# Kernel tuning notes

Hardware: AMD Instinct MI355X
Metric: run time of the kernel (lower is better)

## Reference

```python
import jax, jax.numpy as jnp
import numpy as np

K = 20  # neighbors
DIM = 1024  # args.dim
NCLS = 13  # args.n_classes


def _knn_idx(xt, k):
    # xt: (B,N,C). Torch computes topk of negative squared distances (self included).
    xx = jnp.sum(xt * xt, axis=-1)                       # (B,N)
    inner = jnp.einsum('bnc,bmc->bnm', xt, xt)           # (B,N,N)
    pd = 2.0 * inner - xx[:, :, None] - xx[:, None, :]   # -||xi-xj||^2
    return jax.lax.top_k(pd, k)[1]                       # (B,N,k) int32


def _graph_feature(xt, k):
    # xt: (B,N,C) -> (B,N,k,2C) = concat(neighbor - center, center)
    idx = _knn_idx(xt, k)
    nbr = jax.vmap(lambda a, i: a[i])(xt, idx)           # (B,N,k,C)
    ctr = jnp.broadcast_to(xt[:, :, None, :], nbr.shape)
    return jnp.concatenate([nbr - ctr, ctr], axis=-1)


def _cbl(x, w, s, b):
    # 1x1 conv (no bias) + folded eval-mode BatchNorm (scale s, bias b) + LeakyReLU(0.2)
    y = jnp.einsum('...c,oc->...o', x, w) * s + b
    return jnp.where(y > 0, y, 0.2 * y)


def setup_inputs() -> dict:
    key = jax.random.key(0)
    ks = iter(jax.random.split(key, 64))
    d = {'x': jax.random.normal(next(ks), (8, 3, 4096), jnp.float32)}
    layers = [('1', 64, 6), ('2', 64, 64), ('3', 64, 128), ('4', 64, 64),
              ('5', 64, 128), ('6', DIM, 192), ('8', 256, DIM + 192),
              ('9', 256, 256), ('10', 128, 256)]
    for name, o, i in layers:
        d['w' + name] = jax.random.normal(next(ks), (o, i), jnp.float32) * (1.0 / np.sqrt(i))
        d['s' + name] = jax.random.uniform(next(ks), (o,), jnp.float32, 0.5, 1.5)
        d['b' + name] = jax.random.normal(next(ks), (o,), jnp.float32) * 0.1
    d['w11'] = jax.random.normal(next(ks), (NCLS, 128), jnp.float32) * (1.0 / np.sqrt(128))
    return d


def reference(x, w1, s1, b1, w2, s2, b2, w3, s3, b3, w4, s4, b4,
              w5, s5, b5, w6, s6, b6, w8, s8, b8, w9, s9, b9,
              w10, s10, b10, w11):
    B, _, N = x.shape
    xt = jnp.transpose(x, (0, 2, 1))                      # (B,N,3)

    f = _graph_feature(xt, K)                             # (B,N,k,6)
    f = _cbl(_cbl(f, w1, s1, b1), w2, s2, b2)
    x1 = jnp.max(f, axis=2)                               # (B,N,64)

    f = _graph_feature(x1, K)                             # (B,N,k,128)
    f = _cbl(_cbl(f, w3, s3, b3), w4, s4, b4)
    x2 = jnp.max(f, axis=2)                               # (B,N,64)

    f = _graph_feature(x2, K)
    f = _cbl(f, w5, s5, b5)
    x3 = jnp.max(f, axis=2)                               # (B,N,64)

    cat = jnp.concatenate([x1, x2, x3], axis=-1)          # (B,N,192)
    g = _cbl(cat, w6, s6, b6)                             # (B,N,DIM)
    g = jnp.broadcast_to(jnp.max(g, axis=1, keepdims=True), (B, N, DIM))

    h = jnp.concatenate([g, x1, x2, x3], axis=-1)         # (B,N,DIM+192)
    h = _cbl(h, w8, s8, b8)                               # dropout is eval-mode identity
    h = _cbl(h, w9, s9, b9)
    h = _cbl(h, w10, s10, b10)
    out = jnp.einsum('bnc,oc->bno', h, w11)               # (B,N,NCLS)
    return jnp.transpose(out, (0, 2, 1))                  # (B,NCLS,N)
```

## Files before the change

### kernel.cpp

```cpp
#include <hip/hip_runtime.h>
#include <cstdint>
#include <cstddef>

#define NPTS 4096
#define BATCH 8
#define KNB 20
#define SLOTS 18
#define FLUSH_THR 3

__device__ __forceinline__ float leaky(float v) { return v > 0.f ? v : 0.2f * v; }

__device__ __forceinline__ unsigned encf(float f) {
  unsigned u = __float_as_uint(f);
  return (u & 0x80000000u) ? ~u : (u | 0x80000000u);
}
__device__ __forceinline__ float decf(unsigned e) {
  unsigned u = (e & 0x80000000u) ? (e & 0x7FFFFFFFu) : ~e;
  return __uint_as_float(u);
}

__device__ __forceinline__ unsigned long long mkkey(float pd, int j) {
  unsigned s = encf(pd);
  return (((unsigned long long)(~s)) << 32) | (unsigned)j;
}

__device__ __forceinline__ void tk_insert(float (&hf)[KNB], int (&hj)[KNB], float pd, int j) {
  if (pd > hf[KNB - 1]) {
    float cf = pd;
    int cj = j;
#pragma unroll
    for (int t = 0; t < KNB; ++t) {
      bool gt = cf > hf[t];
      float nf = gt ? cf : hf[t];
      int nj = gt ? cj : hj[t];
      cf = gt ? hf[t] : cf;
      cj = gt ? hj[t] : cj;
      hf[t] = nf;
      hj[t] = nj;
    }
  }
}

#define NEGINF (__int_as_float(0xff800000))

__device__ __forceinline__ void flushbuf(const float* bpd, const unsigned short* bidx, int t, int& cnt, float& thr,
                                         float (&hf)[KNB], int (&hj)[KNB]) {
  for (int s = 0; s < SLOTS; ++s) {
    if (!__any(s < cnt)) break;
    if (s < cnt) {
      float pd = bpd[s * 256 + t];
      int j = bidx[s * 256 + t];
      tk_insert(hf, hj, pd, j);
    }
  }
  cnt = 0;
  thr = hf[KNB - 1];
}

#define APPEND(PD, J)                        \
  do {                                       \
    float _p = (PD);                         \
    if (_p > thr) {                          \
      bpd[cnt * 256 + t] = _p;               \
      bidx[cnt * 256 + t] = (unsigned short)(J); \
      ++cnt;                                 \
    }                                        \
  } while (0)

__device__ __forceinline__ void merge4_out(unsigned long long* mb, int t, const float (&hf)[KNB], const int (&hj)[KNB],
                                           int* __restrict__ op_base) {
#pragma unroll
  for (int s = 0; s < KNB; ++s) mb[(size_t)t * KNB + s] = mkkey(hf[s], hj[s]);
  __syncthreads();
  if ((t & 3) == 0) {
    int p0 = 0, p1 = 0, p2 = 0, p3 = 0;
    const unsigned long long* l0 = mb + (size_t)(t + 0) * KNB;
    const unsigned long long* l1 = mb + (size_t)(t + 1) * KNB;
    const unsigned long long* l2 = mb + (size_t)(t + 2) * KNB;
    const unsigned long long* l3 = mb + (size_t)(t + 3) * KNB;
    for (int s = 0; s < KNB; ++s) {
      unsigned long long u0 = (p0 < KNB) ? l0[p0] : ~0ULL;
      unsigned long long u1 = (p1 < KNB) ? l1[p1] : ~0ULL;
      unsigned long long u2 = (p2 < KNB) ? l2[p2] : ~0ULL;
      unsigned long long u3 = (p3 < KNB) ? l3[p3] : ~0ULL;
      unsigned long long m01 = u0 < u1 ? u0 : u1;
      int s01 = u0 < u1 ? 0 : 1;
      unsigned long long m23 = u2 < u3 ? u2 : u3;
      int s23 = u2 < u3 ? 2 : 3;
      unsigned long long mm = m01 < m23 ? m01 : m23;
      int sm = m01 < m23 ? s01 : s23;
      p0 += (sm == 0);
      p1 += (sm == 1);
      p2 += (sm == 2);
      p3 += (sm == 3);
      op_base[s] = (int)(mm & 0xFFFFFFFFu);
    }
  }
}

__global__ __launch_bounds__(256) void knn_c3(const float* __restrict__ x, int* __restrict__ idxo) {
  __shared__ float smem[11008];
  float4* f4t = (float4*)smem;
  float* bpd = smem + 4096;
  unsigned short* bidx = (unsigned short*)(smem + 8704);
  int b = blockIdx.y, t = threadIdx.x;
  int q = t >> 2, sub = t & 3;
  int i = blockIdx.x * 64 + q;
  const float* xb = x + (size_t)b * 3 * NPTS;
  float qx = xb[i], qy = xb[NPTS + i], qz = xb[2 * NPTS + i];
  float qn = fmaf(qz, qz, fmaf(qy, qy, qx * qx));
  float hf[KNB];
  int hj[KNB];
#pragma unroll
  for (int s = 0; s < KNB; ++s) {
    hf[s] = NEGINF;
    hj[s] = 0x7fffffff;
  }
  float thr = NEGINF;
  int cnt = 0;
  for (int j0 = 0; j0 < NPTS; j0 += 1024) {
    __syncthreads();
#pragma unroll
    for (int l = 0; l < 4; ++l) {
      int p = t + l * 256;
      float px = xb[j0 + p], py = xb[NPTS + j0 + p], pz = xb[2 * NPTS + j0 + p];
      float pn = fmaf(pz, pz, fmaf(py, py, px * px));
      f4t[p] = make_float4(px, py, pz, pn);
    }
    __syncthreads();
    for (int g = 0; g < 16; ++g) {
      if (__any(cnt >= FLUSH_THR)) flushbuf(bpd, bidx, t, cnt, thr, hf, hj);
#pragma unroll
      for (int s = 0; s < 16; ++s) {
        int jj = g * 64 + s * 4 + sub;
        float4 p = f4t[jj];
        float inner = fmaf(p.x, qx, fmaf(p.y, qy, p.z * qz));
        float pd = fmaf(2.0f, inner, -qn) - p.w;
        APPEND(pd, j0 + jj);
      }
    }
  }
  flushbuf(bpd, bidx, t, cnt, thr, hf, hj);
  __syncthreads();
  merge4_out((unsigned long long*)smem, t, hf, hj, idxo + ((size_t)(b * NPTS + i)) * KNB);
}

__global__ __launch_bounds__(256) void rownormk(const float* __restrict__ f, float* __restrict__ nrm) {
  int r = blockIdx.x * 256 + threadIdx.x;
  const float* p = f + (size_t)r * 64;
  float a0 = 0, a1 = 0, a2 = 0, a3 = 0;
#pragma unroll
  for (int c4 = 0; c4 < 16; ++c4) {
    float4 v = *(const float4*)(p + c4 * 4);
    a0 = fmaf(v.x, v.x, a0);
    a1 = fmaf(v.y, v.y, a1);
    a2 = fmaf(v.z, v.z, a2);
    a3 = fmaf(v.w, v.w, a3);
  }
  nrm[r] = (a0 + a1) + (a2 + a3);
}

__global__ __launch_bounds__(256) void knn64g(const float* __restrict__ feat, const float* __restrict__ nrm,
                                              int* __restrict__ idxo) {
  __shared__ float smem[15744];
  float* Qs = smem;
  float* Pp = smem + 4352;
  float* pdt = smem + 4352;
  float* qn_s = smem + 8704;
  float* pn_s = smem + 8768;
  float* bpd = smem + 8832;
  unsigned short* bidx = (unsigned short*)(smem + 13440);
  int b = blockIdx.y, t = threadIdx.x;
  int q0 = blockIdx.x * 64;
  const float* fb = feat + (size_t)b * NPTS * 64;
  const float* nb = nrm + b * NPTS;
  int ty = t >> 4, tx = t & 15;
  int lq = t >> 2, seg = t & 3;

  {
    int r = t >> 2, cs = (t & 3) * 16;
#pragma unroll
    for (int s = 0; s < 4; ++s) {
      float4 v = *(const float4*)(fb + (size_t)(q0 + r) * 64 + cs + s * 4);
      *(float4*)(Qs + r * 68 + cs + s * 4) = v;
    }
    if (t < 64) qn_s[t] = nb[q0 + t];
  }

  float hf[KNB];
  int hj[KNB];
#pragma unroll
  for (int s = 0; s < KNB; ++s) {
    hf[s] = NEGINF;
    hj[s] = 0x7fffffff;
  }
  float thr = NEGINF;
  int cnt = 0;

  for (int j0 = 0; j0 < NPTS; j0 += 64) {
    __syncthreads();
    {
      int j = t >> 2, cs = (t & 3) * 16;
      float* pan = Pp + (j >> 2) * 260 + (j & 3);
#pragma unroll
      for (int s = 0; s < 4; ++s) {
        float4 v = *(const float4*)(fb + (size_t)(j0 + j) * 64 + cs + s * 4);
        pan[(cs + s * 4 + 0) * 4] = v.x;
        pan[(cs + s * 4 + 1) * 4] = v.y;
        pan[(cs + s * 4 + 2) * 4] = v.z;
        pan[(cs + s * 4 + 3) * 4] = v.w;
      }
      if (t < 64) pn_s[t] = nb[j0 + t];
    }
    __syncthreads();
    float acc[4][4];
#pragma unroll
    for (int i = 0; i < 4; ++i)
#pragma unroll
      for (int j = 0; j < 4; ++j) acc[i][j] = 0.f;
    const float* pb = Pp + tx * 260;
#pragma unroll 4
    for (int k4 = 0; k4 < 16; ++k4) {
      float4 Bf0 = *(const float4*)(pb + (k4 * 4 + 0) * 4);
      float4 Bf1 = *(const float4*)(pb + (k4 * 4 + 1) * 4);
      float4 Bf2 = *(const float4*)(pb + (k4 * 4 + 2) * 4);
      float4 Bf3 = *(const float4*)(pb + (k4 * 4 + 3) * 4);
#pragma unroll
      for (int i = 0; i < 4; ++i) {
        float4 Ai = *(const float4*)(Qs + (ty * 4 + i) * 68 + k4 * 4);
        acc[i][0] = fmaf(Ai.x, Bf0.x, acc[i][0]);
        acc[i][1] = fmaf(Ai.x, Bf0.y, acc[i][1]);
        acc[i][2] = fmaf(Ai.x, Bf0.z, acc[i][2]);
        acc[i][3] = fmaf(Ai.x, Bf0.w, acc[i][3]);
        acc[i][0] = fmaf(Ai.y, Bf1.x, acc[i][0]);
        acc[i][1] = fmaf(Ai.y, Bf1.y, acc[i][1]);
        acc[i][2] = fmaf(Ai.y, Bf1.z, acc[i][2]);
        acc[i][3] = fmaf(Ai.y, Bf1.w, acc[i][3]);
        acc[i][0] = fmaf(Ai.z, Bf2.x, acc[i][0]);
        acc[i][1] = fmaf(Ai.z, Bf2.y, acc[i][1]);
        acc[i][2] = fmaf(Ai.z, Bf2.z, acc[i][2]);
        acc[i][3] = fmaf(Ai.z, Bf2.w, acc[i][3]);
        acc[i][0] = fmaf(Ai.w, Bf3.x, acc[i][0]);
        acc[i][1] = fmaf(Ai.w, Bf3.y, acc[i][1]);
        acc[i][2] = fmaf(Ai.w, Bf3.z, acc[i][2]);
        acc[i][3] = fmaf(Ai.w, Bf3.w, acc[i][3]);
      }
    }
    __syncthreads();
#pragma unroll
    for (int i = 0; i < 4; ++i) {
      int qq = ty * 4 + i;
      float qn = qn_s[qq];
      float4 ov;
      ov.x = fmaf(2.f, acc[i][0], -qn) - pn_s[tx * 4 + 0];
      ov.y = fmaf(2.f, acc[i][1], -qn) - pn_s[tx * 4 + 1];
      ov.z = fmaf(2.f, acc[i][2], -qn) - pn_s[tx * 4 + 2];
      ov.w = fmaf(2.f, acc[i][3], -qn) - pn_s[tx * 4 + 3];
      *(float4*)(pdt + qq * 68 + tx * 4) = ov;
    }
    __syncthreads();
    {
      const float* pr = pdt + lq * 68 + seg * 16;
      float4 pv0 = *(const float4*)(pr + 0);
      float4 pv1 = *(const float4*)(pr + 4);
      float4 pv2 = *(const float4*)(pr + 8);
      float4 pv3 = *(const float4*)(pr + 12);
      if (__any(cnt >= FLUSH_THR)) flushbuf(bpd, bidx, t, cnt, thr, hf, hj);
      int jb = j0 + seg * 16;
      APPEND(pv0.x, jb + 0);
      APPEND(pv0.y, jb + 1);
      APPEND(pv0.z, jb + 2);
      APPEND(pv0.w, jb + 3);
      APPEND(pv1.x, jb + 4);
      APPEND(pv1.y, jb + 5);
      APPEND(pv1.z, jb + 6);
      APPEND(pv1.w, jb + 7);
      APPEND(pv2.x, jb + 8);
      APPEND(pv2.y, jb + 9);
      APPEND(pv2.z, jb + 10);
      APPEND(pv2.w, jb + 11);
      APPEND(pv3.x, jb + 12);
      APPEND(pv3.y, jb + 13);
      APPEND(pv3.z, jb + 14);
      APPEND(pv3.w, jb + 15);
    }
  }
  flushbuf(bpd, bidx, t, cnt, thr, hf, hj);
  __syncthreads();
  merge4_out((unsigned long long*)smem, t, hf, hj, idxo + ((size_t)(b * NPTS + q0 + lq)) * KNB);
}

template <int CIN, bool CONV2, bool CHMAJOR>
__global__ __launch_bounds__(256) void edgeconv(const float* __restrict__ src, const int* __restrict__ idx,
                                                const float* __restrict__ w1, const float* __restrict__ s1,
                                                const float* __restrict__ b1, const float* __restrict__ w2,
                                                const float* __restrict__ s2, const float* __restrict__ b2,
                                                float* __restrict__ outp) {
  constexpr int KS = (CIN < 16) ? CIN : 16;
  constexpr int HALF = CIN / 2;
  __shared__ float As[16][84];
  __shared__ float Ws[16][68];
  __shared__ float C1s[80][68];
  __shared__ float W4s[64][68];
  __shared__ float part[16][68];

  int t = threadIdx.x;
  int tx = t & 15, ty = t >> 4;
  int q0 = blockIdx.x * 4;
  int b = q0 >> 12;
  int n0 = q0 & (NPTS - 1);
  const int* idxb = idx + (size_t)q0 * KNB;

  if (CONV2) {
    for (int e = t; e < 64 * 64; e += 256) {
      int o = e >> 6, c = e & 63;
      W4s[c][o] = w2[e];
    }
  }

  float acc1[5][4];
#pragma unroll
  for (int r = 0; r < 5; ++r)
#pragma unroll
    for (int j = 0; j < 4; ++j) acc1[r][j] = 0.f;

  for (int k0 = 0; k0 < CIN; k0 += KS) {
    __syncthreads();
    if (CHMAJOR) {
      const float* sb = src + (size_t)b * 3 * NPTS;
      for (int e = t; e < 80 * KS; e += 256) {
        int row = e / KS, kk = e % KS;
        int nq = row / KNB, k20 = row % KNB;
        int n = n0 + nq;
        int jn2 = idxb[nq * KNB + k20];
        float v;
        if (kk < 3)
          v = sb[kk * NPTS + jn2] - sb[kk * NPTS + n];
        else
          v = sb[(kk - 3) * NPTS + n];
        As[kk][row] = v;
      }
    } else {
      const float* sb = src + (size_t)b * NPTS * 64;
      for (int v4 = t; v4 < 80 * 4; v4 += 256) {
        int row = v4 >> 2, kq = v4 & 3;
        int c = k0 + kq * 4;
        int nq = row / KNB, k20 = row % KNB;
        int n = n0 + nq;
        float4 val;
        if (c < HALF) {
          int jn2 = idxb[nq * KNB + k20];
          float4 nbv = *(const float4*)(sb + (size_t)jn2 * 64 + c);
          float4 ctv = *(const float4*)(sb + (size_t)n * 64 + c);
          val = make_float4(nbv.x - ctv.x, nbv.y - ctv.y, nbv.z - ctv.z, nbv.w - ctv.w);
        } else {
          val = *(const float4*)(sb + (size_t)n * 64 + (c - HALF));
        }
        As[kq * 4 + 0][row] = val.x;
        As[kq * 4 + 1][row] = val.y;
        As[kq * 4 + 2][row] = val.z;
        As[kq * 4 + 3][row] = val.w;
      }
    }
    for (int e = t; e < 64 * KS; e += 256) {
      int o = e / KS, kk = e % KS;
      Ws[kk][o] = w1[o * CIN + k0 + kk];
    }
    __syncthreads();
#pragma unroll
    for (int kk = 0; kk < KS; ++kk) {
      float av[5];
      av[0] = As[kk][ty * 5 + 0];
      av[1] = As[kk][ty * 5 + 1];
      av[2] = As[kk][ty * 5 + 2];
      av[3] = As[kk][ty * 5 + 3];
      av[4] = As[kk][ty * 5 + 4];
      float4 bb = *(const float4*)&Ws[kk][tx * 4];
#pragma unroll
      for (int r = 0; r < 5; ++r) {
        acc1[r][0] = fmaf(av[r], bb.x, acc1[r][0]);
        acc1[r][1] = fmaf(av[r], bb.y, acc1[r][1]);
        acc1[r][2] = fmaf(av[r], bb.z, acc1[r][2]);
        acc1[r][3] = fmaf(av[r], bb.w, acc1[r][3]);
      }
    }
  }
  __syncthreads();
  float4 sv = *(const float4*)(s1 + tx * 4);
  float4 bv = *(const float4*)(b1 + tx * 4);
  float pmax[4];
#pragma unroll
  for (int j = 0; j < 4; ++j) pmax[j] = -3.4e38f;

  if (CONV2) {
#pragma unroll
    for (int r = 0; r < 5; ++r) {
      C1s[ty * 5 + r][tx * 4 + 0] = leaky(fmaf(acc1[r][0], sv.x, bv.x));
      C1s[ty * 5 + r][tx * 4 + 1] = leaky(fmaf(acc1[r][1], sv.y, bv.y));
      C1s[ty * 5 + r][tx * 4 + 2] = leaky(fmaf(acc1[r][2], sv.z, bv.z));
      C1s[ty * 5 + r][tx * 4 + 3] = leaky(fmaf(acc1[r][3], sv.w, bv.w));
    }
    __syncthreads();
    float acc2[5][4];
#pragma unroll
    for (int r = 0; r < 5; ++r)
#pragma unroll
      for (int j = 0; j < 4; ++j) acc2[r][j] = 0.f;
#pragma unroll
    for (int c = 0; c < 64; ++c) {
      float4 wb = *(const float4*)&W4s[c][tx * 4];
      float a0 = C1s[ty * 5 + 0][c];
      float a1 = C1s[ty * 5 + 1][c];
      float a2 = C1s[ty * 5 + 2][c];
      float a3 = C1s[ty * 5 + 3][c];
      float a4 = C1s[ty * 5 + 4][c];
      acc2[0][0] = fmaf(a0, wb.x, acc2[0][0]);
      acc2[0][1] = fmaf(a0, wb.y, acc2[0][1]);
      acc2[0][2] = fmaf(a0, wb.z, acc2[0][2]);
      acc2[0][3] = fmaf(a0, wb.w, acc2[0][3]);
      acc2[1][0] = fmaf(a1, wb.x, acc2[1][0]);
      acc2[1][1] = fmaf(a1, wb.y, acc2[1][1]);
      acc2[1][2] = fmaf(a1, wb.z, acc2[1][2]);
      acc2[1][3] = fmaf(a1, wb.w, acc2[1][3]);
      acc2[2][0] = fmaf(a2, wb.x, acc2[2][0]);
      acc2[2][1] = fmaf(a2, wb.y, acc2[2][1]);
      acc2[2][2] = fmaf(a2, wb.z, acc2[2][2]);
      acc2[2][3] = fmaf(a2, wb.w, acc2[2][3]);
      acc2[3][0] = fmaf(a3, wb.x, acc2[3][0]);
      acc2[3][1] = fmaf(a3, wb.y, acc2[3][1]);
      acc2[3][2] = fmaf(a3, wb.z, acc2[3][2]);
      acc2[3][3] = fmaf(a3, wb.w, acc2[3][3]);
      acc2[4][0] = fmaf(a4, wb.x, acc2[4][0]);
      acc2[4][1] = fmaf(a4, wb.y, acc2[4][1]);
      acc2[4][2] = fmaf(a4, wb.z, acc2[4][2]);
      acc2[4][3] = fmaf(a4, wb.w, acc2[4][3]);
    }
    float4 s2v = *(const float4*)(s2 + tx * 4);
    float4 b2v = *(const float4*)(b2 + tx * 4);
#pragma unroll
    for (int r = 0; r < 5; ++r) {
      pmax[0] = fmaxf(pmax[0], leaky(fmaf(acc2[r][0], s2v.x, b2v.x)));
      pmax[1] = fmaxf(pmax[1], leaky(fmaf(acc2[r][1], s2v.y, b2v.y)));
      pmax[2] = fmaxf(pmax[2], leaky(fmaf(acc2[r][2], s2v.z, b2v.z)));
      pmax[3] = fmaxf(pmax[3], leaky(fmaf(acc2[r][3], s2v.w, b2v.w)));
    }
  } else {
#pragma unroll
    for (int r = 0; r < 5; ++r) {
      pmax[0] = fmaxf(pmax[0], leaky(fmaf(acc1[r][0], sv.x, bv.x)));
      pmax[1] = fmaxf(pmax[1], leaky(fmaf(acc1[r][1], sv.y, bv.y)));
      pmax[2] = fmaxf(pmax[2], leaky(fmaf(acc1[r][2], sv.z, bv.z)));
      pmax[3] = fmaxf(pmax[3], leaky(fmaf(acc1[r][3], sv.w, bv.w)));
    }
  }
  part[ty][tx * 4 + 0] = pmax[0];
  part[ty][tx * 4 + 1] = pmax[1];
  part[ty][tx * 4 + 2] = pmax[2];
  part[ty][tx * 4 + 3] = pmax[3];
  __syncthreads();
  {
    int q = t >> 6, o = t & 63;
    float m = part[q * 4 + 0][o];
    m = fmaxf(m, part[q * 4 + 1][o]);
    m = fmaxf(m, part[q * 4 + 2][o]);
    m = fmaxf(m, part[q * 4 + 3][o]);
    outp[((size_t)(q0 + q)) * 64 + o] = m;
  }
}

#define AM_CAT3 0
#define AM_ROW 1
#define EPI_STORE 0
#define EPI_ADDG 1
#define EPI_MAX 2

template <int AMODE, int EPI>
__global__ __launch_bounds__(256) void gemmk(const float* __restrict__ a0, const float* __restrict__ a1,
                                             const float* __restrict__ a2, const float* __restrict__ w, int ldw,
                                             int Ksz, const float* __restrict__ sc, const float* __restrict__ bi,
                                             const float* __restrict__ gadd, float* __restrict__ outp, int ldo,
                                             unsigned* __restrict__ gmax) {
  __shared__ float As[16][68];
  __shared__ float Bs[16][68];
  int t = threadIdx.x, tx = t & 15, ty = t >> 4;
  int row0 = blockIdx.x * 64;
  int o0 = blockIdx.y * 64;
  float acc[4][4];
#pragma unroll
  for (int i = 0; i < 4; ++i)
#pragma unroll
    for (int j = 0; j < 4; ++j) acc[i][j] = 0.f;
  int arow = t >> 2;
  int ak4 = (t & 3) * 4;
  for (int k0 = 0; k0 < Ksz; k0 += 16) {
    __syncthreads();
    {
      int r = row0 + arow;
      int c = k0 + ak4;
      float4 v;
      if (AMODE == AM_CAT3) {
        const float* s = (c < 64) ? a0 : (c < 128 ? a1 : a2);
        v = *(const float4*)(s + (size_t)r * 64 + (c & 63));
      } else {
        v = *(const float4*)(a0 + (size_t)r * Ksz + c);
      }
      As[ak4 + 0][arow] = v.x;
      As[ak4 + 1][arow] = v.y;
      As[ak4 + 2][arow] = v.z;
      As[ak4 + 3][arow] = v.w;
      float4 wv = *(const float4*)(w + (size_t)(o0 + arow) * ldw + c);
      Bs[ak4 + 0][arow] = wv.x;
      Bs[ak4 + 1][arow] = wv.y;
      Bs[ak4 + 2][arow] = wv.z;
      Bs[ak4 + 3][arow] = wv.w;
    }
    __syncthreads();
#pragma unroll
    for (int kk = 0; kk < 16; ++kk) {
      float4 a = *(const float4*)&As[kk][ty * 4];
      float4 bb = *(const float4*)&Bs[kk][tx * 4];
      acc[0][0] = fmaf(a.x, bb.x, acc[0][0]);
      acc[0][1] = fmaf(a.x, bb.y, acc[0][1]);
      acc[0][2] = fmaf(a.x, bb.z, acc[0][2]);
      acc[0][3] = fmaf(a.x, bb.w, acc[0][3]);
      acc[1][0] = fmaf(a.y, bb.x, acc[1][0]);
      acc[1][1] = fmaf(a.y, bb.y, acc[1][1]);
      acc[1][2] = fmaf(a.y, bb.z, acc[1][2]);
      acc[1][3] = fmaf(a.y, bb.w, acc[1][3]);
      acc[2][0] = fmaf(a.z, bb.x, acc[2][0]);
      acc[2][1] = fmaf(a.z, bb.y, acc[2][1]);
      acc[2][2] = fmaf(a.z, bb.z, acc[2][2]);
      acc[2][3] = fmaf(a.z, bb.w, acc[2][3]);
      acc[3][0] = fmaf(a.w, bb.x, acc[3][0]);
      acc[3][1] = fmaf(a.w, bb.y, acc[3][1]);
      acc[3][2] = fmaf(a.w, bb.z, acc[3][2]);
      acc[3][3] = fmaf(a.w, bb.w, acc[3][3]);
    }
  }
  float4 sv = *(const float4*)(sc + o0 + tx * 4);
  float4 bv = *(const float4*)(bi + o0 + tx * 4);
  if (EPI == EPI_MAX) {
    __syncthreads();
    float pm[4] = {-3.4e38f, -3.4e38f, -3.4e38f, -3.4e38f};
#pragma unroll
    for (int i = 0; i < 4; ++i) {
      pm[0] = fmaxf(pm[0], leaky(fmaf(acc[i][0], sv.x, bv.x)));
      pm[1] = fmaxf(pm[1], leaky(fmaf(acc[i][1], sv.y, bv.y)));
      pm[2] = fmaxf(pm[2], leaky(fmaf(acc[i][2], sv.z, bv.z)));
      pm[3] = fmaxf(pm[3], leaky(fmaf(acc[i][3], sv.w, bv.w)));
    }
    As[ty][tx * 4 + 0] = pm[0];
    As[ty][tx * 4 + 1] = pm[1];
    As[ty][tx * 4 + 2] = pm[2];
    As[ty][tx * 4 + 3] = pm[3];
    __syncthreads();
    if (t < 64) {
      float m = As[0][t];
#pragma unroll
      for (int g = 1; g < 16; ++g) m = fmaxf(m, As[g][t]);
      int b = row0 >> 12;
      atomicMax(&gmax[b * 1024 + o0 + t], encf(m));
    }
  } else {
    float4 ga = make_float4(0.f, 0.f, 0.f, 0.f);
    if (EPI == EPI_ADDG) ga = *(const float4*)(gadd + (row0 >> 12) * 256 + o0 + tx * 4);
#pragma unroll
    for (int i = 0; i < 4; ++i) {
      int r = row0 + ty * 4 + i;
      float4 ov;
      ov.x = leaky(fmaf(acc[i][0] + ga.x, sv.x, bv.x));
      ov.y = leaky(fmaf(acc[i][1] + ga.y, sv.y, bv.y));
      ov.z = leaky(fmaf(acc[i][2] + ga.z, sv.z, bv.z));
      ov.w = leaky(fmaf(acc[i][3] + ga.w, sv.w, bv.w));
      *(float4*)(outp + (size_t)r * ldo + o0 + tx * 4) = ov;
    }
  }
}

__global__ __launch_bounds__(256) void gdotk(const unsigned* __restrict__ gmax, const float* __restrict__ w8,
                                             float* __restrict__ gb8) {
  int wv = blockIdx.x * 4 + (threadIdx.x >> 6);
  int lane = threadIdx.x & 63;
  int b = wv >> 8, o = wv & 255;
  const float* wr = w8 + (size_t)o * 1216;
  const unsigned* gr = gmax + b * 1024;
  float acc = 0.f;
#pragma unroll
  for (int l = 0; l < 4; ++l) {
    int c = lane * 4 + l * 256;
    float4 wv4 = *(const float4*)(wr + c);
    acc = fmaf(decf(gr[c + 0]), wv4.x, acc);
    acc = fmaf(decf(gr[c + 1]), wv4.y, acc);
    acc = fmaf(decf(gr[c + 2]), wv4.z, acc);
    acc = fmaf(decf(gr[c + 3]), wv4.w, acc);
  }
#pragma unroll
  for (int off = 32; off >= 1; off >>= 1) acc += __shfl_down(acc, off);
  if (lane == 0) gb8[b * 256 + o] = acc;
}

__global__ __launch_bounds__(256) void outk(const float* __restrict__ h10, const float* __restrict__ w11,
                                            float* __restrict__ outp) {
  __shared__ float hs[64][132];
  __shared__ float wsm[13][128];
  int b = blockIdx.y, n0 = blockIdx.x * 64, t = threadIdx.x;
  for (int e = t; e < 13 * 128; e += 256) wsm[e >> 7][e & 127] = w11[e];
  const float* hb = h10 + ((size_t)(b * NPTS + n0)) * 128;
#pragma unroll
  for (int l = 0; l < 8; ++l) {
    int v = t + l * 256;
    int row = v >> 5, c4 = (v & 31) * 4;
    *(float4*)(&hs[row][c4]) = *(const float4*)(hb + (size_t)row * 128 + c4);
  }
  __syncthreads();
  for (int e = t; e < 13 * 64; e += 256) {
    int o = e >> 6, n = e & 63;
    float a0 = 0, a1 = 0, a2 = 0, a3 = 0;
#pragma unroll
    for (int c4 = 0; c4 < 32; ++c4) {
      float4 hv = *(const float4*)(&hs[n][c4 * 4]);
      const float* wr = &wsm[o][c4 * 4];
      a0 = fmaf(hv.x, wr[0], a0);
      a1 = fmaf(hv.y, wr[1], a1);
      a2 = fmaf(hv.z, wr[2], a2);
      a3 = fmaf(hv.w, wr[3], a3);
    }
    outp[((size_t)b * 13 + o) * NPTS + n0 + n] = (a0 + a1) + (a2 + a3);
  }
}

extern "C" void kernel_launch(void* const* d_in, const int* in_sizes, int n_in, void* d_out, int out_size, void* d_ws,
                              size_t ws_size, hipStream_t stream) {
  (void)in_sizes;
  (void)n_in;
  (void)out_size;
  (void)ws_size;
  const float* x = (const float*)d_in[0];
  const float* w1 = (const float*)d_in[1];
  const float* s1 = (const float*)d_in[2];
  const float* b1 = (const float*)d_in[3];
  const float* w2 = (const float*)d_in[4];
  const float* s2 = (const float*)d_in[5];
  const float* b2 = (const float*)d_in[6];
  const float* w3 = (const float*)d_in[7];
  const float* s3 = (const float*)d_in[8];
  const float* b3 = (const float*)d_in[9];
  const float* w4 = (const float*)d_in[10];
  const float* s4 = (const float*)d_in[11];
  const float* b4 = (const float*)d_in[12];
  const float* w5 = (const float*)d_in[13];
  const float* s5 = (const float*)d_in[14];
  const float* b5 = (const float*)d_in[15];
  const float* w6 = (const float*)d_in[16];
  const float* s6 = (const float*)d_in[17];
  const float* b6 = (const float*)d_in[18];
  const float* w8 = (const float*)d_in[19];
  const float* s8 = (const float*)d_in[20];
  const float* b8 = (const float*)d_in[21];
  const float* w9 = (const float*)d_in[22];
  const float* s9 = (const float*)d_in[23];
  const float* b9 = (const float*)d_in[24];
  const float* w10 = (const float*)d_in[25];
  const float* s10 = (const float*)d_in[26];
  const float* b10 = (const float*)d_in[27];
  const float* w11 = (const float*)d_in[28];

  float* ws = (float*)d_ws;
  size_t off = 0;
  int* idxb = (int*)ws;
  off += 655360;
  float* x1 = ws + off;
  off += 2097152;
  float* x2 = ws + off;
  off += 2097152;
  float* x3 = ws + off;
  off += 2097152;
  float* nrm = ws + off;
  off += 131072;
  unsigned* gmax = (unsigned*)(ws + off);
  off += 8192;
  float* gb8 = ws + off;
  off += 2048;
  float* h8 = ws + off;
  off += 8388608;
  float* h9 = ws + off;
  off += 8388608;
  float* h10 = h8;
  float* outp = (float*)d_out;

  knn_c3<<<dim3(64, BATCH), 256, 0, stream>>>(x, idxb);
  edgeconv<6, true, true><<<dim3(8192), 256, 0, stream>>>(x, idxb, w1, s1, b1, w2, s2, b2, x1);
  rownormk<<<dim3(128), 256, 0, stream>>>(x1, nrm);
  knn64g<<<dim3(64, BATCH), 256, 0, stream>>>(x1, nrm, idxb);
  edgeconv<128, true, false><<<dim3(8192), 256, 0, stream>>>(x1, idxb, w3, s3, b3, w4, s4, b4, x2);
  rownormk<<<dim3(128), 256, 0, stream>>>(x2, nrm);
  knn64g<<<dim3(64, BATCH), 256, 0, stream>>>(x2, nrm, idxb);
  edgeconv<128, false, false><<<dim3(8192), 256, 0, stream>>>(x2, idxb, w5, s5, b5, nullptr, nullptr, nullptr, x3);
  hipMemsetAsync(gmax, 0, 8192 * sizeof(unsigned), stream);
  gemmk<AM_CAT3, EPI_MAX><<<dim3(512, 16), 256, 0, stream>>>(x1, x2, x3, w6, 192, 192, s6, b6, nullptr, nullptr, 0,
                                                             gmax);
  gdotk<<<dim3(512), 256, 0, stream>>>(gmax, w8, gb8);
  gemmk<AM_CAT3, EPI_ADDG><<<dim3(512, 4), 256, 0, stream>>>(x1, x2, x3, w8 + 1024, 1216, 192, s8, b8, gb8, h8, 256,
                                                             nullptr);
  gemmk<AM_ROW, EPI_STORE><<<dim3(512, 4), 256, 0, stream>>>(h8, nullptr, nullptr, w9, 256, 256, s9, b9, nullptr, h9,
                                                             256, nullptr);
  gemmk<AM_ROW, EPI_STORE><<<dim3(512, 2), 256, 0, stream>>>(h9, nullptr, nullptr, w10, 256, 256, s10, b10, nullptr,
                                                             h10, 128, nullptr);
  outk<<<dim3(64, BATCH), 256, 0, stream>>>(h10, w11, outp);
}
```

Baseline: 2.463 ms.

## Factor edge convs into per-point U/V GEMMs and retile kNN distance kernel

The first edge conv is rewritten algebraically: W·[xj−xi, xi] = W_a·xj + (W_b−W_a)·xi. Per-point U and V projections are computed once by small GEMMs (or uv3 for the 3-channel input), and the edge kernels only gather U rows, add V, and apply the epilogue and max. This removes the per-edge first-layer matmul over all K neighbours. The kNN kernel moves to 128 threads with an 8x8 register tile over 128-point tiles, an XOR-swizzled distance buffer and smaller candidate buffers, and the xyz kNN re-tunes its flush cadence. This costs extra U/V workspace traffic and may change register pressure and occupancy.

```diff
diff --git a/kernel.cpp b/kernel.cpp
--- a/kernel.cpp
+++ b/kernel.cpp
@@ -5,8 +5,7 @@
 #define NPTS 4096
 #define BATCH 8
 #define KNB 20
-#define SLOTS 18
-#define FLUSH_THR 3
+#define SLOTS 12
 
 __device__ __forceinline__ float leaky(float v) { return v > 0.f ? v : 0.2f * v; }
 
@@ -23,6 +22,8 @@
   unsigned s = encf(pd);
   return (((unsigned long long)(~s)) << 32) | (unsigned)j;
 }
+
+#define NEGINF (__int_as_float(0xff800000))
 
 __device__ __forceinline__ void tk_insert(float (&hf)[KNB], int (&hj)[KNB], float pd, int j) {
   if (pd > hf[KNB - 1]) {
@@ -41,15 +42,13 @@
   }
 }
 
-#define NEGINF (__int_as_float(0xff800000))
-
-__device__ __forceinline__ void flushbuf(const float* bpd, const unsigned short* bidx, int t, int& cnt, float& thr,
-                                         float (&hf)[KNB], int (&hj)[KNB]) {
+__device__ __forceinline__ void flushbuf(const float* bpd, const unsigned short* bidx, int t, int stride, int& cnt,
+                                         float& thr, float (&hf)[KNB], int (&hj)[KNB]) {
   for (int s = 0; s < SLOTS; ++s) {
     if (!__any(s < cnt)) break;
     if (s < cnt) {
-      float pd = bpd[s * 256 + t];
-      int j = bidx[s * 256 + t];
+      float pd = bpd[s * stride + t];
+      int j = bidx[s * stride + t];
       tk_insert(hf, hj, pd, j);
     }
   }
@@ -57,27 +56,71 @@
   thr = hf[KNB - 1];
 }
 
-#define APPEND(PD, J)                        \
-  do {                                       \
-    float _p = (PD);                         \
-    if (_p > thr) {                          \
-      bpd[cnt * 256 + t] = _p;               \
-      bidx[cnt * 256 + t] = (unsigned short)(J); \
-      ++cnt;                                 \
-    }                                        \
+#define APPEND(PD, J, STRIDE)                    \
+  do {                                           \
+    float _p = (PD);                             \
+    if (_p > thr) {                              \
+      bpd[cnt * (STRIDE) + t] = _p;              \
+      bidx[cnt * (STRIDE) + t] = (unsigned short)(J); \
+      ++cnt;                                     \
+    }                                            \
   } while (0)
 
-__device__ __forceinline__ void merge4_out(unsigned long long* mb, int t, const float (&hf)[KNB], const int (&hj)[KNB],
-                                           int* __restrict__ op_base) {
+__global__ __launch_bounds__(256) void knn_c3(const float* __restrict__ x, int* __restrict__ idxo) {
+  __shared__ __align__(16) float smem[11008];
+  float4* f4t = (float4*)smem;
+  float* bpd = smem + 4096;
+  unsigned short* bidx = (unsigned short*)(smem + 8704);
+  int b = blockIdx.y, t = threadIdx.x;
+  int q = t >> 2, sub = t & 3;
+  int i = blockIdx.x * 64 + q;
+  const float* xb = x + (size_t)b * 3 * NPTS;
+  float qx = xb[i], qy = xb[NPTS + i], qz = xb[2 * NPTS + i];
+  float qn = fmaf(qz, qz, fmaf(qy, qy, qx * qx));
+  float hf[KNB];
+  int hj[KNB];
+#pragma unroll
+  for (int s = 0; s < KNB; ++s) {
+    hf[s] = NEGINF;
+    hj[s] = 0x7fffffff;
+  }
+  float thr = NEGINF;
+  int cnt = 0;
+  for (int j0 = 0; j0 < NPTS; j0 += 1024) {
+    __syncthreads();
+#pragma unroll
+    for (int l = 0; l < 4; ++l) {
+      int p = t + l * 256;
+      float px = xb[j0 + p], py = xb[NPTS + j0 + p], pz = xb[2 * NPTS + j0 + p];
+      float pn = fmaf(pz, pz, fmaf(py, py, px * px));
+      f4t[p] = make_float4(px, py, pz, pn);
+    }
+    __syncthreads();
+    for (int g = 0; g < 32; ++g) {
+      if (__any(cnt >= 5)) flushbuf(bpd, bidx, t, 256, cnt, thr, hf, hj);
+#pragma unroll
+      for (int s = 0; s < 8; ++s) {
+        int jj = g * 32 + s * 4 + sub;
+        float4 p = f4t[jj];
+        float inner = fmaf(p.x, qx, fmaf(p.y, qy, p.z * qz));
+        float pd = fmaf(2.0f, inner, -qn) - p.w;
+        APPEND(pd, j0 + jj, 256);
+      }
+    }
+  }
+  flushbuf(bpd, bidx, t, 256, cnt, thr, hf, hj);
+  __syncthreads();
+  unsigned long long* mb = (unsigned long long*)smem;
 #pragma unroll
   for (int s = 0; s < KNB; ++s) mb[(size_t)t * KNB + s] = mkkey(hf[s], hj[s]);
   __syncthreads();
-  if ((t & 3) == 0) {
+  if (sub == 0) {
     int p0 = 0, p1 = 0, p2 = 0, p3 = 0;
     const unsigned long long* l0 = mb + (size_t)(t + 0) * KNB;
     const unsigned long long* l1 = mb + (size_t)(t + 1) * KNB;
     const unsigned long long* l2 = mb + (size_t)(t + 2) * KNB;
     const unsigned long long* l3 = mb + (size_t)(t + 3) * KNB;
+    int* op = idxo + ((size_t)(b * NPTS + i)) * KNB;
     for (int s = 0; s < KNB; ++s) {
       unsigned long long u0 = (p0 < KNB) ? l0[p0] : ~0ULL;
       unsigned long long u1 = (p1 < KNB) ? l1[p1] : ~0ULL;
@@ -93,56 +136,9 @@
       p1 += (sm == 1);
       p2 += (sm == 2);
       p3 += (sm == 3);
-      op_base[s] = (int)(mm & 0xFFFFFFFFu);
-    }
-  }
-}
-
-__global__ __launch_bounds__(256) void knn_c3(const float* __restrict__ x, int* __restrict__ idxo) {
-  __shared__ float smem[11008];
-  float4* f4t = (float4*)smem;
-  float* bpd = smem + 4096;
-  unsigned short* bidx = (unsigned short*)(smem + 8704);
-  int b = blockIdx.y, t = threadIdx.x;
-  int q = t >> 2, sub = t & 3;
-  int i = blockIdx.x * 64 + q;
-  const float* xb = x + (size_t)b * 3 * NPTS;
-  float qx = xb[i], qy = xb[NPTS + i], qz = xb[2 * NPTS + i];
-  float qn = fmaf(qz, qz, fmaf(qy, qy, qx * qx));
-  float hf[KNB];
-  int hj[KNB];
-#pragma unroll
-  for (int s = 0; s < KNB; ++s) {
-    hf[s] = NEGINF;
-    hj[s] = 0x7fffffff;
-  }
-  float thr = NEGINF;
-  int cnt = 0;
-  for (int j0 = 0; j0 < NPTS; j0 += 1024) {
-    __syncthreads();
-#pragma unroll
-    for (int l = 0; l < 4; ++l) {
-      int p = t + l * 256;
-      float px = xb[j0 + p], py = xb[NPTS + j0 + p], pz = xb[2 * NPTS + j0 + p];
-      float pn = fmaf(pz, pz, fmaf(py, py, px * px));
-      f4t[p] = make_float4(px, py, pz, pn);
-    }
-    __syncthreads();
-    for (int g = 0; g < 16; ++g) {
-      if (__any(cnt >= FLUSH_THR)) flushbuf(bpd, bidx, t, cnt, thr, hf, hj);
-#pragma unroll
-      for (int s = 0; s < 16; ++s) {
-        int jj = g * 64 + s * 4 + sub;
-        float4 p = f4t[jj];
-        float inner = fmaf(p.x, qx, fmaf(p.y, qy, p.z * qz));
-        float pd = fmaf(2.0f, inner, -qn) - p.w;
-        APPEND(pd, j0 + jj);
-      }
-    }
-  }
-  flushbuf(bpd, bidx, t, cnt, thr, hf, hj);
-  __syncthreads();
-  merge4_out((unsigned long long*)smem, t, hf, hj, idxo + ((size_t)(b * NPTS + i)) * KNB);
+      op[s] = (int)(mm & 0xFFFFFFFFu);
+    }
+  }
 }
 
 __global__ __launch_bounds__(256) void rownormk(const float* __restrict__ f, float* __restrict__ nrm) {
@@ -160,33 +156,32 @@
   nrm[r] = (a0 + a1) + (a2 + a3);
 }
 
-__global__ __launch_bounds__(256) void knn64g(const float* __restrict__ feat, const float* __restrict__ nrm,
+__global__ __launch_bounds__(128) void knn64g(const float* __restrict__ feat, const float* __restrict__ nrm,
                                               int* __restrict__ idxo) {
-  __shared__ float smem[15744];
-  float* Qs = smem;
-  float* Pp = smem + 4352;
-  float* pdt = smem + 4352;
-  float* qn_s = smem + 8704;
-  float* pn_s = smem + 8768;
-  float* bpd = smem + 8832;
-  unsigned short* bidx = (unsigned short*)(smem + 13440);
+  __shared__ __align__(16) float smem[15360];
+  float* Qt = smem;
+  float* Pt = smem + 4352;
+  float* pdt = smem + 8576;
+  float* pn_s = smem + 12928;
+  float* bpd = smem + 13056;
+  unsigned short* bidx = (unsigned short*)(smem + 13056 + SLOTS * 128);
   int b = blockIdx.y, t = threadIdx.x;
   int q0 = blockIdx.x * 64;
   const float* fb = feat + (size_t)b * NPTS * 64;
   const float* nb = nrm + b * NPTS;
-  int ty = t >> 4, tx = t & 15;
-  int lq = t >> 2, seg = t & 3;
+  int tx = t & 15, ty = t >> 4;
 
   {
-    int r = t >> 2, cs = (t & 3) * 16;
-#pragma unroll
-    for (int s = 0; s < 4; ++s) {
-      float4 v = *(const float4*)(fb + (size_t)(q0 + r) * 64 + cs + s * 4);
-      *(float4*)(Qs + r * 68 + cs + s * 4) = v;
-    }
-    if (t < 64) qn_s[t] = nb[q0 + t];
-  }
-
+    int q = t >> 1, kh = (t & 1) * 32;
+#pragma unroll
+    for (int s = 0; s < 8; ++s) {
+      float4 v = *(const float4*)(fb + (size_t)(q0 + q) * 64 + kh + s * 4);
+      Qt[(kh + s * 4 + 0) * 68 + q] = v.x;
+      Qt[(kh + s * 4 + 1) * 68 + q] = v.y;
+      Qt[(kh + s * 4 + 2) * 68 + q] = v.z;
+      Qt[(kh + s * 4 + 3) * 68 + q] = v.w;
+    }
+  }
   float hf[KNB];
   int hj[KNB];
 #pragma unroll
@@ -197,275 +192,263 @@
   float thr = NEGINF;
   int cnt = 0;
 
-  for (int j0 = 0; j0 < NPTS; j0 += 64) {
-    __syncthreads();
-    {
-      int j = t >> 2, cs = (t & 3) * 16;
-      float* pan = Pp + (j >> 2) * 260 + (j & 3);
-#pragma unroll
-      for (int s = 0; s < 4; ++s) {
-        float4 v = *(const float4*)(fb + (size_t)(j0 + j) * 64 + cs + s * 4);
-        pan[(cs + s * 4 + 0) * 4] = v.x;
-        pan[(cs + s * 4 + 1) * 4] = v.y;
-        pan[(cs + s * 4 + 2) * 4] = v.z;
-        pan[(cs + s * 4 + 3) * 4] = v.w;
+  for (int j0 = 0; j0 < NPTS; j0 += 128) {
+    float acc[8][8];
+#pragma unroll
+    for (int i = 0; i < 8; ++i)
+#pragma unroll
+      for (int j = 0; j < 8; ++j) acc[i][j] = 0.f;
+
+    for (int kp = 0; kp < 2; ++kp) {
+      __syncthreads();
+      int kg = kp * 32;
+#pragma unroll
+      for (int s = 0; s < 8; ++s) {
+        int j = (t >> 2) + (s & 3) * 32;
+        int c = (t & 3) * 8 + (s >> 2) * 4;
+        float4 v = *(const float4*)(fb + (size_t)(j0 + j) * 64 + kg + c);
+        Pt[(c + 0) * 132 + j] = v.x;
+        Pt[(c + 1) * 132 + j] = v.y;
+        Pt[(c + 2) * 132 + j] = v.z;
+        Pt[(c + 3) * 132 + j] = v.w;
       }
-      if (t < 64) pn_s[t] = nb[j0 + t];
-    }
-    __syncthreads();
-    float acc[4][4];
-#pragma unroll
-    for (int i = 0; i < 4; ++i)
-#pragma unroll
-      for (int j = 0; j < 4; ++j) acc[i][j] = 0.f;
-    const float* pb = Pp + tx * 260;
+      if (kp == 0) pn_s[t] = nb[j0 + t];
+      __syncthreads();
 #pragma unroll 4
-    for (int k4 = 0; k4 < 16; ++k4) {
-      float4 Bf0 = *(const float4*)(pb + (k4 * 4 + 0) * 4);
-      float4 Bf1 = *(const float4*)(pb + (k4 * 4 + 1) * 4);
-      float4 Bf2 = *(const float4*)(pb + (k4 * 4 + 2) * 4);
-      float4 Bf3 = *(const float4*)(pb + (k4 * 4 + 3) * 4);
-#pragma unroll
-      for (int i = 0; i < 4; ++i) {
-        float4 Ai = *(const float4*)(Qs + (ty * 4 + i) * 68 + k4 * 4);
-        acc[i][0] = fmaf(Ai.x, Bf0.x, acc[i][0]);
-        acc[i][1] = fmaf(Ai.x, Bf0.y, acc[i][1]);
-        acc[i][2] = fmaf(Ai.x, Bf0.z, acc[i][2]);
-        acc[i][3] = fmaf(Ai.x, Bf0.w, acc[i][3]);
-        acc[i][0] = fmaf(Ai.y, Bf1.x, acc[i][0]);
-        acc[i][1] = fmaf(Ai.y, Bf1.y, acc[i][1]);
-        acc[i][2] = fmaf(Ai.y, Bf1.z, acc[i][2]);
-        acc[i][3] = fmaf(Ai.y, Bf1.w, acc[i][3]);
-        acc[i][0] = fmaf(Ai.z, Bf2.x, acc[i][0]);
-        acc[i][1] = fmaf(Ai.z, Bf2.y, acc[i][1]);
-        acc[i][2] = fmaf(Ai.z, Bf2.z, acc[i][2]);
-        acc[i][3] = fmaf(Ai.z, Bf2.w, acc[i][3]);
-        acc[i][0] = fmaf(Ai.w, Bf3.x, acc[i][0]);
-        acc[i][1] = fmaf(Ai.w, Bf3.y, acc[i][1]);
-        acc[i][2] = fmaf(Ai.w, Bf3.z, acc[i][2]);
-        acc[i][3] = fmaf(Ai.w, Bf3.w, acc[i][3]);
+      for (int k = 0; k < 32; ++k) {
+        float4 A0 = *(const float4*)(Qt + (kg + k) * 68 + ty * 4);
+        float4 A1 = *(const float4*)(Qt + (kg + k) * 68 + 32 + ty * 4);
+        float4 B0 = *(const float4*)(Pt + k * 132 + tx * 4);
+        float4 B1 = *(const float4*)(Pt + k * 132 + 64 + tx * 4);
+        float Aa[8] = {A0.x, A0.y, A0.z, A0.w, A1.x, A1.y, A1.z, A1.w};
+        float Bb[8] = {B0.x, B0.y, B0.z, B0.w, B1.x, B1.y, B1.z, B1.w};
+#pragma unroll
+        for (int i = 0; i < 8; ++i)
+#pragma unroll
+          for (int j = 0; j < 8; ++j) acc[i][j] = fmaf(Aa[i], Bb[j], acc[i][j]);
       }
     }
-    __syncthreads();
-#pragma unroll
-    for (int i = 0; i < 4; ++i) {
-      int qq = ty * 4 + i;
-      float qn = qn_s[qq];
-      float4 ov;
-      ov.x = fmaf(2.f, acc[i][0], -qn) - pn_s[tx * 4 + 0];
-      ov.y = fmaf(2.f, acc[i][1], -qn) - pn_s[tx * 4 + 1];
-      ov.z = fmaf(2.f, acc[i][2], -qn) - pn_s[tx * 4 + 2];
-      ov.w = fmaf(2.f, acc[i][3], -qn) - pn_s[tx * 4 + 3];
-      *(float4*)(pdt + qq * 68 + tx * 4) = ov;
-    }
-    __syncthreads();
-    {
-      const float* pr = pdt + lq * 68 + seg * 16;
-      float4 pv0 = *(const float4*)(pr + 0);
-      float4 pv1 = *(const float4*)(pr + 4);
-      float4 pv2 = *(const float4*)(pr + 8);
-      float4 pv3 = *(const float4*)(pr + 12);
-      if (__any(cnt >= FLUSH_THR)) flushbuf(bpd, bidx, t, cnt, thr, hf, hj);
-      int jb = j0 + seg * 16;
-      APPEND(pv0.x, jb + 0);
-      APPEND(pv0.y, jb + 1);
-      APPEND(pv0.z, jb + 2);
-      APPEND(pv0.w, jb + 3);
-      APPEND(pv1.x, jb + 4);
-      APPEND(pv1.y, jb + 5);
-      APPEND(pv1.z, jb + 6);
-      APPEND(pv1.w, jb + 7);
-      APPEND(pv2.x, jb + 8);
-      APPEND(pv2.y, jb + 9);
-      APPEND(pv2.z, jb + 10);
-      APPEND(pv2.w, jb + 11);
-      APPEND(pv3.x, jb + 12);
-      APPEND(pv3.y, jb + 13);
-      APPEND(pv3.z, jb + 14);
-      APPEND(pv3.w, jb + 15);
-    }
-  }
-  flushbuf(bpd, bidx, t, cnt, thr, hf, hj);
-  __syncthreads();
-  merge4_out((unsigned long long*)smem, t, hf, hj, idxo + ((size_t)(b * NPTS + q0 + lq)) * KNB);
-}
-
-template <int CIN, bool CONV2, bool CHMAJOR>
-__global__ __launch_bounds__(256) void edgeconv(const float* __restrict__ src, const int* __restrict__ idx,
-                                                const float* __restrict__ w1, const float* __restrict__ s1,
+#pragma unroll
+    for (int jh = 0; jh < 2; ++jh) {
+      __syncthreads();
+      float4 pnv = *(const float4*)(pn_s + jh * 64 + tx * 4);
+#pragma unroll
+      for (int qa = 0; qa < 2; ++qa)
+#pragma unroll
+        for (int qi = 0; qi < 4; ++qi) {
+          int row = qa * 32 + ty * 4 + qi;
+          int key = (row >> 3) & 3;
+          float4 v;
+          v.x = fmaf(2.f, acc[qa * 4 + qi][jh * 4 + 0], -pnv.x);
+          v.y = fmaf(2.f, acc[qa * 4 + qi][jh * 4 + 1], -pnv.y);
+          v.z = fmaf(2.f, acc[qa * 4 + qi][jh * 4 + 2], -pnv.z);
+          v.w = fmaf(2.f, acc[qa * 4 + qi][jh * 4 + 3], -pnv.w);
+          *(float4*)(pdt + row * 68 + ((tx * 4) ^ (key << 2))) = v;
+        }
+      __syncthreads();
+      {
+        int lq = t >> 1, seg = t & 1;
+        int key = (lq >> 3) & 3;
+        const float* pr = pdt + lq * 68;
+        int jb = j0 + jh * 64 + seg * 32;
+#pragma unroll
+        for (int ep = 0; ep < 4; ++ep) {
+          if (__any(cnt >= 5)) flushbuf(bpd, bidx, t, 128, cnt, thr, hf, hj);
+#pragma unroll
+          for (int e2 = 0; e2 < 2; ++e2) {
+            int e = ep * 2 + e2;
+            float4 pv = *(const float4*)(pr + ((seg * 32 + e * 4) ^ (key << 2)));
+            APPEND(pv.x, jb + e * 4 + 0, 128);
+            APPEND(pv.y, jb + e * 4 + 1, 128);
+            APPEND(pv.z, jb + e * 4 + 2, 128);
+            APPEND(pv.w, jb + e * 4 + 3, 128);
+          }
+        }
+      }
+    }
+  }
+  flushbuf(bpd, bidx, t, 128, cnt, thr, hf, hj);
+  __syncthreads();
+  unsigned long long* mb = (unsigned long long*)smem;
+#pragma unroll
+  for (int s = 0; s < KNB; ++s) mb[(size_t)t * KNB + s] = mkkey(hf[s], hj[s]);
+  __syncthreads();
+  if ((t & 1) == 0) {
+    int p0 = 0, p1 = 0;
+    const unsigned long long* l0 = mb + (size_t)(t + 0) * KNB;
+    const unsigned long long* l1 = mb + (size_t)(t + 1) * KNB;
+    int* op = idxo + ((size_t)(b * NPTS + q0 + (t >> 1))) * KNB;
+    for (int s = 0; s < KNB; ++s) {
+      unsigned long long u0 = (p0 < KNB) ? l0[p0] : ~0ULL;
+      unsigned long long u1 = (p1 < KNB) ? l1[p1] : ~0ULL;
+      bool t0 = u0 < u1;
+      unsigned long long mm = t0 ? u0 : u1;
+      p0 += t0;
+      p1 += !t0;
+      op[s] = (int)(mm & 0xFFFFFFFFu);
+    }
+  }
+}
+
+__global__ __launch_bounds__(256) void uv3(const float* __restrict__ x, const float* __restrict__ w1,
+                                           float* __restrict__ U, float* __restrict__ V) {
+  __shared__ float xs[64][3];
+  __shared__ float wa[192], wv[192];
+  int t = threadIdx.x;
+  int g0 = blockIdx.x * 64;
+  if (t < 192) {
+    int o = t / 3, c = t % 3;
+    float a = w1[o * 6 + c];
+    wa[t] = a;
+    wv[t] = w1[o * 6 + 3 + c] - a;
+  }
+  if (t < 192) {
+    int c = t >> 6, i = t & 63;
+    int b = g0 >> 12, n0 = g0 & (NPTS - 1);
+    xs[i][c] = x[(size_t)b * 3 * NPTS + c * NPTS + n0 + i];
+  }
+  __syncthreads();
+  int nl = t >> 2, cq = t & 3;
+  float x0 = xs[nl][0], x1v = xs[nl][1], x2v = xs[nl][2];
+  size_t ob = (size_t)(g0 + nl) * 64 + cq * 16;
+#pragma unroll
+  for (int s = 0; s < 4; ++s) {
+    float4 u, v;
+    float* up = (float*)&u;
+    float* vp = (float*)&v;
+#pragma unroll
+    for (int e = 0; e < 4; ++e) {
+      int o = cq * 16 + s * 4 + e;
+      up[e] = fmaf(x2v, wa[o * 3 + 2], fmaf(x1v, wa[o * 3 + 1], x0 * wa[o * 3]));
+      vp[e] = fmaf(x2v, wv[o * 3 + 2], fmaf(x1v, wv[o * 3 + 1], x0 * wv[o * 3]));
+    }
+    *(float4*)(U + ob + s * 4) = u;
+    *(float4*)(V + ob + s * 4) = v;
+  }
+}
+
+__global__ __launch_bounds__(256) void edgemax2(const float* __restrict__ U, const float* __restrict__ V,
+                                                const int* __restrict__ idx, const float* __restrict__ s1,
                                                 const float* __restrict__ b1, const float* __restrict__ w2,
                                                 const float* __restrict__ s2, const float* __restrict__ b2,
                                                 float* __restrict__ outp) {
-  constexpr int KS = (CIN < 16) ? CIN : 16;
-  constexpr int HALF = CIN / 2;
-  __shared__ float As[16][84];
-  __shared__ float Ws[16][68];
-  __shared__ float C1s[80][68];
+  __shared__ __align__(16) float E1s[160][68];
   __shared__ float W4s[64][68];
-  __shared__ float part[16][68];
-
+  __shared__ int jrow[160];
+  int t = threadIdx.x, tx = t & 15, ty = t >> 4;
+  int q0 = blockIdx.x * 8;
+  const float* Ub = U + (((size_t)(q0 >> 12)) << 12) * 64;
+  for (int e = t; e < 4096; e += 256) W4s[e & 63][e >> 6] = w2[e];
+  if (t < 160) jrow[t] = idx[(size_t)q0 * KNB + t];
+  __syncthreads();
+  for (int v = t; v < 160 * 16; v += 256) {
+    int row = v >> 4, cq = (v & 15) * 4;
+    int q = (row * 205) >> 12;
+    int j = jrow[row];
+    float4 uv = *(const float4*)(Ub + (size_t)j * 64 + cq);
+    float4 vv = *(const float4*)(V + ((size_t)(q0 + q)) * 64 + cq);
+    float4 s1v = *(const float4*)(s1 + cq);
+    float4 b1v = *(const float4*)(b1 + cq);
+    float4 ev;
+    ev.x = leaky(fmaf(uv.x + vv.x, s1v.x, b1v.x));
+    ev.y = leaky(fmaf(uv.y + vv.y, s1v.y, b1v.y));
+    ev.z = leaky(fmaf(uv.z + vv.z, s1v.z, b1v.z));
+    ev.w = leaky(fmaf(uv.w + vv.w, s1v.w, b1v.w));
+    *(float4*)(&E1s[row][cq]) = ev;
+  }
+  __syncthreads();
+  float acc[10][4];
+#pragma unroll
+  for (int r = 0; r < 10; ++r)
+#pragma unroll
+    for (int j = 0; j < 4; ++j) acc[r][j] = 0.f;
+#pragma unroll 2
+  for (int k4 = 0; k4 < 16; ++k4) {
+    float4 B0 = *(const float4*)(&W4s[k4 * 4 + 0][tx * 4]);
+    float4 B1 = *(const float4*)(&W4s[k4 * 4 + 1][tx * 4]);
+    float4 B2 = *(const float4*)(&W4s[k4 * 4 + 2][tx * 4]);
+    float4 B3 = *(const float4*)(&W4s[k4 * 4 + 3][tx * 4]);
+#pragma unroll
+    for (int r = 0; r < 10; ++r) {
+      float4 a = *(const float4*)(&E1s[ty * 10 + r][k4 * 4]);
+      acc[r][0] = fmaf(a.w, B3.x, fmaf(a.z, B2.x, fmaf(a.y, B1.x, fmaf(a.x, B0.x, acc[r][0]))));
+      acc[r][1] = fmaf(a.w, B3.y, fmaf(a.z, B2.y, fmaf(a.y, B1.y, fmaf(a.x, B0.y, acc[r][1]))));
+      acc[r][2] = fmaf(a.w, B3.z, fmaf(a.z, B2.z, fmaf(a.y, B1.z, fmaf(a.x, B0.z, acc[r][2]))));
+      acc[r][3] = fmaf(a.w, B3.w, fmaf(a.z, B2.w, fmaf(a.y, B1.w, fmaf(a.x, B0.w, acc[r][3]))));
+    }
+  }
+  __syncthreads();
+  float* part = (float*)E1s;
+  float4 s2v = *(const float4*)(s2 + tx * 4);
+  float4 b2v = *(const float4*)(b2 + tx * 4);
+  float pm[4] = {-3.4e38f, -3.4e38f, -3.4e38f, -3.4e38f};
+#pragma unroll
+  for (int r = 0; r < 10; ++r) {
+    pm[0] = fmaxf(pm[0], leaky(fmaf(acc[r][0], s2v.x, b2v.x)));
+    pm[1] = fmaxf(pm[1], leaky(fmaf(acc[r][1], s2v.y, b2v.y)));
+    pm[2] = fmaxf(pm[2], leaky(fmaf(acc[r][2], s2v.z, b2v.z)));
+    pm[3] = fmaxf(pm[3], leaky(fmaf(acc[r][3], s2v.w, b2v.w)));
+  }
+  part[ty * 68 + tx * 4 + 0] = pm[0];
+  part[ty * 68 + tx * 4 + 1] = pm[1];
+  part[ty * 68 + tx * 4 + 2] = pm[2];
+  part[ty * 68 + tx * 4 + 3] = pm[3];
+  __syncthreads();
+  {
+    int e = t;
+#pragma unroll
+    for (int l = 0; l < 2; ++l) {
+      int q = e >> 6, o = e & 63;
+      float m = fmaxf(part[(2 * q) * 68 + o], part[(2 * q + 1) * 68 + o]);
+      outp[((size_t)(q0 + q)) * 64 + o] = m;
+      e += 256;
+    }
+  }
+}
+
+__global__ __launch_bounds__(256) void edgemax1(const float* __restrict__ U, const float* __restrict__ V,
+                                                const int* __restrict__ idx, const float* __restrict__ s1,
+                                                const float* __restrict__ b1, float* __restrict__ outp) {
   int t = threadIdx.x;
-  int tx = t & 15, ty = t >> 4;
-  int q0 = blockIdx.x * 4;
-  int b = q0 >> 12;
-  int n0 = q0 & (NPTS - 1);
-  const int* idxb = idx + (size_t)q0 * KNB;
-
-  if (CONV2) {
-    for (int e = t; e < 64 * 64; e += 256) {
-      int o = e >> 6, c = e & 63;
-      W4s[c][o] = w2[e];
-    }
-  }
-
-  float acc1[5][4];
-#pragma unroll
-  for (int r = 0; r < 5; ++r)
-#pragma unroll
-    for (int j = 0; j < 4; ++j) acc1[r][j] = 0.f;
-
-  for (int k0 = 0; k0 < CIN; k0 += KS) {
-    __syncthreads();
-    if (CHMAJOR) {
-      const float* sb = src + (size_t)b * 3 * NPTS;
-      for (int e = t; e < 80 * KS; e += 256) {
-        int row = e / KS, kk = e % KS;
-        int nq = row / KNB, k20 = row % KNB;
-        int n = n0 + nq;
-        int jn2 = idxb[nq * KNB + k20];
-        float v;
-        if (kk < 3)
-          v = sb[kk * NPTS + jn2] - sb[kk * NPTS + n];
-        else
-          v = sb[(kk - 3) * NPTS + n];
-        As[kk][row] = v;
-      }
-    } else {
-      const float* sb = src + (size_t)b * NPTS * 64;
-      for (int v4 = t; v4 < 80 * 4; v4 += 256) {
-        int row = v4 >> 2, kq = v4 & 3;
-        int c = k0 + kq * 4;
-        int nq = row / KNB, k20 = row % KNB;
-        int n = n0 + nq;
-        float4 val;
-        if (c < HALF) {
-          int jn2 = idxb[nq * KNB + k20];
-          float4 nbv = *(const float4*)(sb + (size_t)jn2 * 64 + c);
-          float4 ctv = *(const float4*)(sb + (size_t)n * 64 + c);
-          val = make_float4(nbv.x - ctv.x, nbv.y - ctv.y, nbv.z - ctv.z, nbv.w - ctv.w);
-        } else {
-          val = *(const float4*)(sb + (size_t)n * 64 + (c - HALF));
-        }
-        As[kq * 4 + 0][row] = val.x;
-        As[kq * 4 + 1][row] = val.y;
-        As[kq * 4 + 2][row] = val.z;
-        As[kq * 4 + 3][row] = val.w;
-      }
-    }
-    for (int e = t; e < 64 * KS; e += 256) {
-      int o = e / KS, kk = e % KS;
-      Ws[kk][o] = w1[o * CIN + k0 + kk];
-    }
-    __syncthreads();
-#pragma unroll
-    for (int kk = 0; kk < KS; ++kk) {
-      float av[5];
-      av[0] = As[kk][ty * 5 + 0];
-      av[1] = As[kk][ty * 5 + 1];
-      av[2] = As[kk][ty * 5 + 2];
-      av[3] = As[kk][ty * 5 + 3];
-      av[4] = As[kk][ty * 5 + 4];
-      float4 bb = *(const float4*)&Ws[kk][tx * 4];
-#pragma unroll
-      for (int r = 0; r < 5; ++r) {
-        acc1[r][0] = fmaf(av[r], bb.x, acc1[r][0]);
-        acc1[r][1] = fmaf(av[r], bb.y, acc1[r][1]);
-        acc1[r][2] = fmaf(av[r], bb.z, acc1[r][2]);
-        acc1[r][3] = fmaf(av[r], bb.w, acc1[r][3]);
-      }
-    }
-  }
-  __syncthreads();
-  float4 sv = *(const float4*)(s1 + tx * 4);
-  float4 bv = *(const float4*)(b1 + tx * 4);
-  float pmax[4];
-#pragma unroll
-  for (int j = 0; j < 4; ++j) pmax[j] = -3.4e38f;
-
-  if (CONV2) {
-#pragma unroll
-    for (int r = 0; r < 5; ++r) {
-      C1s[ty * 5 + r][tx * 4 + 0] = leaky(fmaf(acc1[r][0], sv.x, bv.x));
-      C1s[ty * 5 + r][tx * 4 + 1] = leaky(fmaf(acc1[r][1], sv.y, bv.y));
-      C1s[ty * 5 + r][tx * 4 + 2] = leaky(fmaf(acc1[r][2], sv.z, bv.z));
-      C1s[ty * 5 + r][tx * 4 + 3] = leaky(fmaf(acc1[r][3], sv.w, bv.w));
-    }
-    __syncthreads();
-    float acc2[5][4];
-#pragma unroll
-    for (int r = 0; r < 5; ++r)
-#pragma unroll
-      for (int j = 0; j < 4; ++j) acc2[r][j] = 0.f;
-#pragma unroll
-    for (int c = 0; c < 64; ++c) {
-      float4 wb = *(const float4*)&W4s[c][tx * 4];
-      float a0 = C1s[ty * 5 + 0][c];
-      float a1 = C1s[ty * 5 + 1][c];
-      float a2 = C1s[ty * 5 + 2][c];
-      float a3 = C1s[ty * 5 + 3][c];
-      float a4 = C1s[ty * 5 + 4][c];
-      acc2[0][0] = fmaf(a0, wb.x, acc2[0][0]);
-      acc2[0][1] = fmaf(a0, wb.y, acc2[0][1]);
-      acc2[0][2] = fmaf(a0, wb.z, acc2[0][2]);
-      acc2[0][3] = fmaf(a0, wb.w, acc2[0][3]);
-      acc2[1][0] = fmaf(a1, wb.x, acc2[1][0]);
-      acc2[1][1] = fmaf(a1, wb.y, acc2[1][1]);
-      acc2[1][2] = fmaf(a1, wb.z, acc2[1][2]);
-      acc2[1][3] = fmaf(a1, wb.w, acc2[1][3]);
-      acc2[2][0] = fmaf(a2, wb.x, acc2[2][0]);
-      acc2[2][1] = fmaf(a2, wb.y, acc2[2][1]);
-      acc2[2][2] = fmaf(a2, wb.z, acc2[2][2]);
-      acc2[2][3] = fmaf(a2, wb.w, acc2[2][3]);
-      acc2[3][0] = fmaf(a3, wb.x, acc2[3][0]);
-      acc2[3][1] = fmaf(a3, wb.y, acc2[3][1]);
-      acc2[3][2] = fmaf(a3, wb.z, acc2[3][2]);
-      acc2[3][3] = fmaf(a3, wb.w, acc2[3][3]);
-      acc2[4][0] = fmaf(a4, wb.x, acc2[4][0]);
-      acc2[4][1] = fmaf(a4, wb.y, acc2[4][1]);
-      acc2[4][2] = fmaf(a4, wb.z, acc2[4][2]);
-      acc2[4][3] = fmaf(a4, wb.w, acc2[4][3]);
-    }
-    float4 s2v = *(const float4*)(s2 + tx * 4);
-    float4 b2v = *(const float4*)(b2 + tx * 4);
-#pragma unroll
-    for (int r = 0; r < 5; ++r) {
-      pmax[0] = fmaxf(pmax[0], leaky(fmaf(acc2[r][0], s2v.x, b2v.x)));
-      pmax[1] = fmaxf(pmax[1], leaky(fmaf(acc2[r][1], s2v.y, b2v.y)));
-      pmax[2] = fmaxf(pmax[2], leaky(fmaf(acc2[r][2], s2v.z, b2v.z)));
-      pmax[3] = fmaxf(pmax[3], leaky(fmaf(acc2[r][3], s2v.w, b2v.w)));
-    }
-  } else {
-#pragma unroll
-    for (int r = 0; r < 5; ++r) {
-      pmax[0] = fmaxf(pmax[0], leaky(fmaf(acc1[r][0], sv.x, bv.x)));
-      pmax[1] = fmaxf(pmax[1], leaky(fmaf(acc1[r][1], sv.y, bv.y)));
-      pmax[2] = fmaxf(pmax[2], leaky(fmaf(acc1[r][2], sv.z, bv.z)));
-      pmax[3] = fmaxf(pmax[3], leaky(fmaf(acc1[r][3], sv.w, bv.w)));
-    }
-  }
-  part[ty][tx * 4 + 0] = pmax[0];
-  part[ty][tx * 4 + 1] = pmax[1];
-  part[ty][tx * 4 + 2] = pmax[2];
-  part[ty][tx * 4 + 3] = pmax[3];
-  __syncthreads();
-  {
-    int q = t >> 6, o = t & 63;
-    float m = part[q * 4 + 0][o];
-    m = fmaxf(m, part[q * 4 + 1][o]);
-    m = fmaxf(m, part[q * 4 + 2][o]);
-    m = fmaxf(m, part[q * 4 + 3][o]);
-    outp[((size_t)(q0 + q)) * 64 + o] = m;
-  }
+  int g = blockIdx.x * 64 + (t >> 2);
+  const float* Ub = U + (((size_t)(g >> 12)) << 12) * 64;
+  int cs = (t & 3) * 16;
+  const float* vr = V + (size_t)g * 64 + cs;
+  float4 v0 = *(const float4*)(vr + 0), v1 = *(const float4*)(vr + 4);
+  float4 v2 = *(const float4*)(vr + 8), v3 = *(const float4*)(vr + 12);
+  float4 s0 = *(const float4*)(s1 + cs + 0), s1v = *(const float4*)(s1 + cs + 4);
+  float4 s2v = *(const float4*)(s1 + cs + 8), s3v = *(const float4*)(s1 + cs + 12);
+  float4 b0 = *(const float4*)(b1 + cs + 0), b1v = *(const float4*)(b1 + cs + 4);
+  float4 b2v = *(const float4*)(b1 + cs + 8), b3v = *(const float4*)(b1 + cs + 12);
+  float4 m0 = make_float4(-3.4e38f, -3.4e38f, -3.4e38f, -3.4e38f), m1 = m0, m2 = m0, m3 = m0;
+  const int* ib = idx + (size_t)g * KNB;
+  for (int k = 0; k < KNB; ++k) {
+    int j = ib[k];
+    const float* ur = Ub + (size_t)j * 64 + cs;
+    float4 u0 = *(const float4*)(ur + 0), u1 = *(const float4*)(ur + 4);
+    float4 u2 = *(const float4*)(ur + 8), u3 = *(const float4*)(ur + 12);
+    m0.x = fmaxf(m0.x, leaky(fmaf(u0.x + v0.x, s0.x, b0.x)));
+    m0.y = fmaxf(m0.y, leaky(fmaf(u0.y + v0.y, s0.y, b0.y)));
+    m0.z = fmaxf(m0.z, leaky(fmaf(u0.z + v0.z, s0.z, b0.z)));
+    m0.w = fmaxf(m0.w, leaky(fmaf(u0.w + v0.w, s0.w, b0.w)));
+    m1.x = fmaxf(m1.x, leaky(fmaf(u1.x + v1.x, s1v.x, b1v.x)));
+    m1.y = fmaxf(m1.y, leaky(fmaf(u1.y + v1.y, s1v.y, b1v.y)));
+    m1.z = fmaxf(m1.z, leaky(fmaf(u1.z + v1.z, s1v.z, b1v.z)));
+    m1.w = fmaxf(m1.w, leaky(fmaf(u1.w + v1.w, s1v.w, b1v.w)));
+    m2.x = fmaxf(m2.x, leaky(fmaf(u2.x + v2.x, s2v.x, b2v.x)));
+    m2.y = fmaxf(m2.y, leaky(fmaf(u2.y + v2.y, s2v.y, b2v.y)));
+    m2.z = fmaxf(m2.z, leaky(fmaf(u2.z + v2.z, s2v.z, b2v.z)));
+    m2.w = fmaxf(m2.w, leaky(fmaf(u2.w + v2.w, s2v.w, b2v.w)));
+    m3.x = fmaxf(m3.x, leaky(fmaf(u3.x + v3.x, s3v.x, b3v.x)));
+    m3.y = fmaxf(m3.y, leaky(fmaf(u3.y + v3.y, s3v.y, b3v.y)));
+    m3.z = fmaxf(m3.z, leaky(fmaf(u3.z + v3.z, s3v.z, b3v.z)));
+    m3.w = fmaxf(m3.w, leaky(fmaf(u3.w + v3.w, s3v.w, b3v.w)));
+  }
+  float* orow = outp + (size_t)g * 64 + cs;
+  *(float4*)(orow + 0) = m0;
+  *(float4*)(orow + 4) = m1;
+  *(float4*)(orow + 8) = m2;
+  *(float4*)(orow + 12) = m3;
 }
 
 #define AM_CAT3 0
@@ -473,8 +456,9 @@
 #define EPI_STORE 0
 #define EPI_ADDG 1
 #define EPI_MAX 2
-
-template <int AMODE, int EPI>
+#define EPI_RAW 3
+
+template <int AMODE, int EPI, int BSUB>
 __global__ __launch_bounds__(256) void gemmk(const float* __restrict__ a0, const float* __restrict__ a1,
                                              const float* __restrict__ a2, const float* __restrict__ w, int ldw,
                                              int Ksz, const float* __restrict__ sc, const float* __restrict__ bi,
@@ -509,6 +493,10 @@
       As[ak4 + 2][arow] = v.z;
       As[ak4 + 3][arow] = v.w;
       float4 wv = *(const float4*)(w + (size_t)(o0 + arow) * ldw + c);
+      if (BSUB) {
+        float4 w2v = *(const float4*)(w + (size_t)(o0 + arow) * ldw + Ksz + c);
+        wv = make_float4(w2v.x - wv.x, w2v.y - wv.y, w2v.z - wv.z, w2v.w - wv.w);
+      }
       Bs[ak4 + 0][arow] = wv.x;
       Bs[ak4 + 1][arow] = wv.y;
       Bs[ak4 + 2][arow] = wv.z;
@@ -537,8 +525,11 @@
       acc[3][3] = fmaf(a.w, bb.w, acc[3][3]);
     }
   }
-  float4 sv = *(const float4*)(sc + o0 + tx * 4);
-  float4 bv = *(const float4*)(bi + o0 + tx * 4);
+  float4 sv = make_float4(0.f, 0.f, 0.f, 0.f), bv = sv;
+  if (EPI != EPI_RAW) {
+    sv = *(const float4*)(sc + o0 + tx * 4);
+    bv = *(const float4*)(bi + o0 + tx * 4);
+  }
   if (EPI == EPI_MAX) {
     __syncthreads();
     float pm[4] = {-3.4e38f, -3.4e38f, -3.4e38f, -3.4e38f};
@@ -560,6 +551,13 @@
       for (int g = 1; g < 16; ++g) m = fmaxf(m, As[g][t]);
       int b = row0 >> 12;
       atomicMax(&gmax[b * 1024 + o0 + t], encf(m));
+    }
+  } else if (EPI == EPI_RAW) {
+#pragma unroll
+    for (int i = 0; i < 4; ++i) {
+      int r = row0 + ty * 4 + i;
+      float4 ov = make_float4(acc[i][0], acc[i][1], acc[i][2], acc[i][3]);
+      *(float4*)(outp + (size_t)r * ldo + o0 + tx * 4) = ov;
     }
   } else {
     float4 ga = make_float4(0.f, 0.f, 0.f, 0.f);
@@ -686,25 +684,36 @@
   float* h9 = ws + off;
   off += 8388608;
   float* h10 = h8;
+  float* U = h9;
+  float* V = h9 + 2097152;
   float* outp = (float*)d_out;
 
   knn_c3<<<dim3(64, BATCH), 256, 0, stream>>>(x, idxb);
-  edgeconv<6, true, true><<<dim3(8192), 256, 0, stream>>>(x, idxb, w1, s1, b1, w2, s2, b2, x1);
+  uv3<<<dim3(512), 256, 0, stream>>>(x, w1, U, V);
+  edgemax2<<<dim3(4096), 256, 0, stream>>>(U, V, idxb, s1, b1, w2, s2, b2, x1);
   rownormk<<<dim3(128), 256, 0, stream>>>(x1, nrm);
-  knn64g<<<dim3(64, BATCH), 256, 0, stream>>>(x1, nrm, idxb);
-  edgeconv<128, true, false><<<dim3(8192), 256, 0, stream>>>(x1, idxb, w3, s3, b3, w4, s4, b4, x2);
+  knn64g<<<dim3(64, BATCH), 128, 0, stream>>>(x1, nrm, idxb);
+  gemmk<AM_ROW, EPI_RAW, 0><<<dim3(512, 1), 256, 0, stream>>>(x1, nullptr, nullptr, w3, 128, 64, nullptr, nullptr,
+                                                              nullptr, U, 64, nullptr);
+  gemmk<AM_ROW, EPI_RAW, 1><<<dim3(512, 1), 256, 0, stream>>>(x1, nullptr, nullptr, w3, 128, 64, nullptr, nullptr,
+                                                              nullptr, V, 64, nullptr);
+  edgemax2<<<dim3(4096), 256, 0, stream>>>(U, V, idxb, s3, b3, w4, s4, b4, x2);
   rownormk<<<dim3(128), 256, 0, stream>>>(x2, nrm);
-  knn64g<<<dim3(64, BATCH), 256, 0, stream>>>(x2, nrm, idxb);
-  edgeconv<128, false, false><<<dim3(8192), 256, 0, stream>>>(x2, idxb, w5, s5, b5, nullptr, nullptr, nullptr, x3);
+  knn64g<<<dim3(64, BATCH), 128, 0, stream>>>(x2, nrm, idxb);
+  gemmk<AM_ROW, EPI_RAW, 0><<<dim3(512, 1), 256, 0, stream>>>(x2, nullptr, nullptr, w5, 128, 64, nullptr, nullptr,
+                                                              nullptr, U, 64, nullptr);
+  gemmk<AM_ROW, EPI_RAW, 1><<<dim3(512, 1), 256, 0, stream>>>(x2, nullptr, nullptr, w5, 128, 64, nullptr, nullptr,
+                                                              nullptr, V, 64, nullptr);
+  edgemax1<<<dim3(512), 256, 0, stream>>>(U, V, idxb, s5, b5, x3);
   hipMemsetAsync(gmax, 0, 8192 * sizeof(unsigned), stream);
-  gemmk<AM_CAT3, EPI_MAX><<<dim3(512, 16), 256, 0, stream>>>(x1, x2, x3, w6, 192, 192, s6, b6, nullptr, nullptr, 0,
-                                                             gmax);
+  gemmk<AM_CAT3, EPI_MAX, 0><<<dim3(512, 16), 256, 0, stream>>>(x1, x2, x3, w6, 192, 192, s6, b6, nullptr, nullptr, 0,
+                                                                gmax);
   gdotk<<<dim3(512), 256, 0, stream>>>(gmax, w8, gb8);
-  gemmk<AM_CAT3, EPI_ADDG><<<dim3(512, 4), 256, 0, stream>>>(x1, x2, x3, w8 + 1024, 1216, 192, s8, b8, gb8, h8, 256,
-                                                             nullptr);
-  gemmk<AM_ROW, EPI_STORE><<<dim3(512, 4), 256, 0, stream>>>(h8, nullptr, nullptr, w9, 256, 256, s9, b9, nullptr, h9,
-                                                             256, nullptr);
-  gemmk<AM_ROW, EPI_STORE><<<dim3(512, 2), 256, 0, stream>>>(h9, nullptr, nullptr, w10, 256, 256, s10, b10, nullptr,
-                                                             h10, 128, nullptr);
+  gemmk<AM_CAT3, EPI_ADDG, 0><<<dim3(512, 4), 256, 0, stream>>>(x1, x2, x3, w8 + 1024, 1216, 192, s8, b8, gb8, h8, 256,
+                                                                nullptr);
+  gemmk<AM_ROW, EPI_STORE, 0><<<dim3(512, 4), 256, 0, stream>>>(h8, nullptr, nullptr, w9, 256, 256, s9, b9, nullptr,
+                                                                h9, 256, nullptr);
+  gemmk<AM_ROW, EPI_STORE, 0><<<dim3(512, 2), 256, 0, stream>>>(h9, nullptr, nullptr, w10, 256, 256, s10, b10, nullptr,
+                                                                h10, 128, nullptr);
   outk<<<dim3(64, BATCH), 256, 0, stream>>>(h10, w11, outp);
 }
```

Result: faster. 2.094 ms (-14.9%).
